# Kernel tuning notes

Hardware: AMD Instinct MI355X
Metric: run time of the kernel (lower is better)

## Reference

```python
import jax, jax.numpy as jnp
import numpy as np

N, E, G = 100000, 1600000, 128
IN_DIM, H, C = 329, 4, 64
NEG_SLOPE = 0.2


def setup_inputs() -> dict:
    key = jax.random.key(0)
    ks = jax.random.split(key, 12)
    x = jax.random.normal(ks[0], (N, IN_DIM), dtype=jnp.float32)
    edge_index = jax.random.randint(ks[1], (2, E), 0, N, dtype=jnp.int64)
    batch = jnp.sort(jax.random.randint(ks[2], (N,), 0, G, dtype=jnp.int64))
    s = 1.0 / np.sqrt(IN_DIM)
    W = jax.random.uniform(ks[3], (IN_DIM, H * C), jnp.float32, -s, s)
    att_src = jax.random.normal(ks[4], (H, C), dtype=jnp.float32) * 0.1
    att_dst = jax.random.normal(ks[5], (H, C), dtype=jnp.float32) * 0.1
    bias = jnp.zeros((C,), jnp.float32)
    s1 = 1.0 / np.sqrt(C)
    w1 = jax.random.uniform(ks[6], (C, 64), jnp.float32, -s1, s1)
    b1 = jnp.zeros((64,), jnp.float32)
    s2 = 1.0 / np.sqrt(64)
    w2 = jax.random.uniform(ks[7], (64, 1), jnp.float32, -s2, s2)
    b2 = jnp.zeros((1,), jnp.float32)
    return {"x": x, "W": W, "att_src": att_src, "att_dst": att_dst,
            "bias": bias, "w1": w1, "b1": b1, "w2": w2, "b2": b2,
            "edge_index": edge_index, "batch": batch}


def reference(x, W, att_src, att_dst, bias, w1, b1, w2, b2, edge_index, batch):
    # --- GATConv (heads=4, concat=False, add_self_loops=True) ---
    xp = (x @ W).reshape(N, H, C)                       # [N,H,C]
    a_src = jnp.einsum('nhc,hc->nh', xp, att_src)       # [N,H]
    a_dst = jnp.einsum('nhc,hc->nh', xp, att_dst)       # [N,H]
    loops = jnp.arange(N, dtype=edge_index.dtype)
    src = jnp.concatenate([edge_index[0], loops])       # [E+N]
    dst = jnp.concatenate([edge_index[1], loops])
    logits = jax.nn.leaky_relu(a_src[src] + a_dst[dst], NEG_SLOPE)  # [E+N,H]
    # segment softmax over edges sharing a destination
    mx = jax.ops.segment_max(logits, dst, num_segments=N)
    ex = jnp.exp(logits - mx[dst])
    denom = jax.ops.segment_sum(ex, dst, num_segments=N)
    alpha = ex / denom[dst]                             # [E+N,H]
    msg = xp[src] * alpha[:, :, None]                   # [E+N,H,C]
    agg = jax.ops.segment_sum(msg, dst, num_segments=N) # [N,H,C]
    h = jax.nn.relu(agg.mean(axis=1) + bias)            # [N,C]
    # --- global mean pool over graphs ---
    counts = jax.ops.segment_sum(jnp.ones((N,), h.dtype), batch, num_segments=G)
    g = jax.ops.segment_sum(h, batch, num_segments=G) / jnp.maximum(counts, 1.0)[:, None]
    # --- head MLP ---
    y = jax.nn.sigmoid(jax.nn.relu(g @ w1 + b1) @ w2 + b2)  # [G,1]
    return y
```

## Files before the change

### kernel.cpp

```cpp
#include <hip/hip_runtime.h>
#include <math.h>

#define N_NODES 100000
#define N_EDGES 1600000
#define N_GRAPHS 128
#define IN_DIM 329
#define NH 4
#define CC 64
#define HC 256
#define NEG_SLOPE 0.2f

#define K_PAD 384
#define M_PAD 100096
#define NBUCK 196
#define BCAP 10240
#define EPB 4096

typedef unsigned short u16;
typedef unsigned char u8;
typedef unsigned int u32;
typedef __attribute__((ext_vector_type(8))) short short8;
typedef __attribute__((ext_vector_type(4))) float floatx4;
typedef __attribute__((ext_vector_type(2))) float floatx2;

__device__ __forceinline__ u16 f2bf(float f) {
    u32 u = __float_as_uint(f);
    u32 r = (u + 0x7FFFu + ((u >> 16) & 1u)) >> 16;
    return (u16)r;
}

__device__ __forceinline__ u8 f2fp8(float f) {
#if __has_builtin(__builtin_amdgcn_cvt_pk_fp8_f32)
    int pk = __builtin_amdgcn_cvt_pk_fp8_f32(f, f, 0, false);
    return (u8)(pk & 0xFF);
#else
    u32 u = __float_as_uint(f);
    u32 sgn = (u >> 24) & 0x80;
    float af = fabsf(f);
    if (af >= 448.f) return (u8)(sgn | 0x7E);
    if (af < 0.015625f) {
        int m = (int)rintf(af * 512.f);
        if (m >= 8) return (u8)(sgn | 0x08);
        return (u8)(sgn | (u32)m);
    }
    u32 au = u & 0x7FFFFFFF;
    u32 r = au + 0x0007FFFFu + ((au >> 20) & 1u);
    u32 e = r >> 23;
    u32 m3 = (r >> 20) & 7;
    int fe = (int)e - 127 + 7;
    if (fe >= 16) return (u8)(sgn | 0x7E);
    return (u8)(sgn | ((u32)fe << 3) | m3);
#endif
}

__device__ __forceinline__ float fp82f_sw(u32 b) {
    u32 s = (b & 0x80u) << 24;
    u32 e = (b >> 3) & 0xF;
    u32 m = b & 7;
    if (e == 0) {
        float v = (float)m * 0.001953125f;
        return (b & 0x80) ? -v : v;
    }
    return __uint_as_float(s | ((e + 120) << 23) | (m << 20));
}

__device__ __forceinline__ floatx4 dec4(int p) {
#if __has_builtin(__builtin_amdgcn_cvt_pk_f32_fp8)
    floatx2 lo = __builtin_amdgcn_cvt_pk_f32_fp8(p, false);
    floatx2 hi = __builtin_amdgcn_cvt_pk_f32_fp8(p, true);
    floatx4 r; r.x = lo.x; r.y = lo.y; r.z = hi.x; r.w = hi.y;
    return r;
#else
    floatx4 r;
    r.x = fp82f_sw(p & 0xFF);  r.y = fp82f_sw((p >> 8) & 0xFF);
    r.z = fp82f_sw((p >> 16) & 0xFF); r.w = fp82f_sw((p >> 24) & 0xFF);
    return r;
#endif
}

__device__ __forceinline__ void async_copy16(const void* g, void* l) {
    __builtin_amdgcn_global_load_lds((const __attribute__((address_space(1))) void*)g,
                                     (__attribute__((address_space(3))) void*)l, 16, 0, 0);
}

__device__ __forceinline__ float sel4(float4 a, int h) {
    float lo = (h & 1) ? a.y : a.x;
    float hi = (h & 1) ? a.w : a.z;
    return (h & 2) ? hi : lo;
}

__global__ __launch_bounds__(256) void convert_kernel(
    const float* __restrict__ x, const float* __restrict__ W,
    u16* __restrict__ xb, u16* __restrict__ WbT)
{
    const int xslots = M_PAD * (K_PAD / 4);
    int t = blockIdx.x * 256 + threadIdx.x;
    if (t < xslots) {
        int row = t / 96;
        int slot = t - row * 96;
        int k0 = slot * 4;
        ushort4 o = {0, 0, 0, 0};
        if (row < N_NODES) {
            const float* xr = x + (size_t)row * IN_DIM + k0;
            if (k0 + 3 < IN_DIM) {
                o.x = f2bf(xr[0]); o.y = f2bf(xr[1]); o.z = f2bf(xr[2]); o.w = f2bf(xr[3]);
            } else {
                if (k0 < IN_DIM)     o.x = f2bf(xr[0]);
                if (k0 + 1 < IN_DIM) o.y = f2bf(xr[1]);
                if (k0 + 2 < IN_DIM) o.z = f2bf(xr[2]);
            }
        }
        *(ushort4*)(xb + (size_t)row * K_PAD + k0) = o;
    } else {
        int i = t - xslots;
        if (i >= HC * 96) return;
        int c = i / 96;
        int slot = i - c * 96;
        int k0 = slot * 4;
        ushort4 o = {0, 0, 0, 0};
        const float* wp = W + c;
        if (k0 < IN_DIM)     o.x = f2bf(wp[(size_t)k0 * HC]);
        if (k0 + 1 < IN_DIM) o.y = f2bf(wp[(size_t)(k0 + 1) * HC]);
        if (k0 + 2 < IN_DIM) o.z = f2bf(wp[(size_t)(k0 + 2) * HC]);
        if (k0 + 3 < IN_DIM) o.w = f2bf(wp[(size_t)(k0 + 3) * HC]);
        *(ushort4*)(WbT + (size_t)c * K_PAD + k0) = o;
    }
}

__global__ __launch_bounds__(256) void gemm_mfma_kernel(
    const u16* __restrict__ xb, const u16* __restrict__ WbT,
    const float* __restrict__ att_src, const float* __restrict__ att_dst,
    u8* __restrict__ xp8, float* __restrict__ a_src, float* __restrict__ a_dst)
{
    __shared__ u16 As[128 * 64];
    __shared__ u16 Bs[128 * 64];

    const int tid = threadIdx.x;
    const int lane = tid & 63;
    const int wave = tid >> 6;
    const int lr = lane & 15;
    const int q = lane >> 4;
    const int row0 = blockIdx.x * 128;
    const int col0 = blockIdx.y * 128;
    const int rm0 = (wave & 1) * 64;
    const int cn0 = (wave >> 1) * 64;

    floatx4 acc[4][4];
#pragma unroll
    for (int i = 0; i < 4; i++)
#pragma unroll
        for (int j = 0; j < 4; j++) {
            acc[i][j].x = 0.f; acc[i][j].y = 0.f; acc[i][j].z = 0.f; acc[i][j].w = 0.f;
        }

    for (int k0 = 0; k0 < K_PAD; k0 += 64) {
#pragma unroll
        for (int t = 0; t < 4; t++) {
            int off = (tid + t * 256) * 16;
            int row = off >> 7;
            int col = off & 127;
            int gcol = col ^ ((row & 7) * 16);
            const char* ga = (const char*)xb + (size_t)(row0 + row) * (K_PAD * 2) + k0 * 2 + gcol;
            async_copy16(ga, (char*)As + off);
            const char* gb = (const char*)WbT + (size_t)(col0 + row) * (K_PAD * 2) + k0 * 2 + gcol;
            async_copy16(gb, (char*)Bs + off);
        }
        __syncthreads();

        short8 af[2][4], bf[2][4];
#pragma unroll
        for (int ks = 0; ks < 2; ks++) {
#pragma unroll
            for (int i = 0; i < 4; i++) {
                int ra = rm0 + i * 16 + lr;
                int ca = (ks * 64 + q * 16) ^ ((ra & 7) * 16);
                af[ks][i] = *(const short8*)((const char*)As + ra * 128 + ca);
                int rb = cn0 + i * 16 + lr;
                int cb = (ks * 64 + q * 16) ^ ((rb & 7) * 16);
                bf[ks][i] = *(const short8*)((const char*)Bs + rb * 128 + cb);
            }
        }
#pragma unroll
        for (int ks = 0; ks < 2; ks++)
#pragma unroll
            for (int i = 0; i < 4; i++)
#pragma unroll
                for (int j = 0; j < 4; j++)
                    acc[i][j] = __builtin_amdgcn_mfma_f32_16x16x32_bf16(af[ks][i], bf[ks][j], acc[i][j], 0, 0, 0);
        __syncthreads();
    }

    const int h_w = (col0 + cn0) >> 6;
    float asj[4], adj[4];
#pragma unroll
    for (int j = 0; j < 4; j++) {
        asj[j] = att_src[h_w * 64 + j * 16 + lr];
        adj[j] = att_dst[h_w * 64 + j * 16 + lr];
    }
#pragma unroll
    for (int i = 0; i < 4; i++) {
        float psv[4] = {0, 0, 0, 0}, pdv[4] = {0, 0, 0, 0};
#pragma unroll
        for (int j = 0; j < 4; j++) {
            int col = col0 + cn0 + j * 16 + lr;
            float v[4] = {acc[i][j].x, acc[i][j].y, acc[i][j].z, acc[i][j].w};
#pragma unroll
            for (int r = 0; r < 4; r++) {
                psv[r] = fmaf(v[r], asj[j], psv[r]);
                pdv[r] = fmaf(v[r], adj[j], pdv[r]);
                int row = row0 + rm0 + i * 16 + q * 4 + r;
                if (row < N_NODES) xp8[(size_t)row * HC + col] = f2fp8(v[r]);
            }
        }
#pragma unroll
        for (int m = 1; m < 16; m <<= 1) {
#pragma unroll
            for (int r = 0; r < 4; r++) {
                psv[r] += __shfl_xor(psv[r], m, 64);
                pdv[r] += __shfl_xor(pdv[r], m, 64);
            }
        }
        if (lr == 0) {
#pragma unroll
            for (int r = 0; r < 4; r++) {
                int row = row0 + rm0 + i * 16 + q * 4 + r;
                if (row < N_NODES) {
                    a_src[row * 4 + h_w] = psv[r];
                    a_dst[row * 4 + h_w] = pdv[r];
                }
            }
        }
    }
}

__global__ __launch_bounds__(256) void bin2_kernel(
    const int* __restrict__ ei, int* __restrict__ bcur, int2* __restrict__ bins)
{
    __shared__ int hist[NBUCK];
    __shared__ int lofs[NBUCK];
    __shared__ int gpos[NBUCK];
    __shared__ int lcur[NBUCK];
    __shared__ int sc[256];
    __shared__ int2 lbuf[EPB];

    const int t = threadIdx.x;
    const int lo = blockIdx.x * EPB;
    const int hi = min(lo + EPB, N_EDGES + N_NODES);

    for (int b = t; b < NBUCK; b += 256) hist[b] = 0;
    __syncthreads();

    for (int i = lo + t; i < hi; i += 256) {
        int d = (i < N_EDGES) ? ei[N_EDGES + i] : (i - N_EDGES);
        atomicAdd(&hist[d >> 9], 1);
    }
    __syncthreads();

    int v = (t < NBUCK) ? hist[t] : 0;
    sc[t] = v;
    __syncthreads();
    for (int off = 1; off < 256; off <<= 1) {
        int u = (t >= off) ? sc[t - off] : 0;
        __syncthreads();
        sc[t] += u;
        __syncthreads();
    }
    if (t < NBUCK) {
        int excl = sc[t] - v;
        lofs[t] = excl;
        lcur[t] = excl;
        gpos[t] = atomicAdd(&bcur[t], v);
    }
    __syncthreads();

    for (int i = lo + t; i < hi; i += 256) {
        int s, d;
        if (i < N_EDGES) { s = ei[i]; d = ei[N_EDGES + i]; }
        else             { s = i - N_EDGES; d = s; }
        int b = d >> 9;
        int pos = atomicAdd(&lcur[b], 1);
        int2 r; r.x = s; r.y = d;
        lbuf[pos] = r;
    }
    __syncthreads();

    int total = hi - lo;
    for (int i = t; i < total; i += 256) {
        int2 r = lbuf[i];
        int b = r.y >> 9;
        int ob = gpos[b] + (i - lofs[b]);
        if (ob < BCAP) bins[(size_t)b * BCAP + ob] = r;
    }
}

__global__ __launch_bounds__(256) void fill3_kernel(
    const int* __restrict__ bcur, const int2* __restrict__ bins,
    int2* __restrict__ rs_deg, int* __restrict__ csr)
{
    __shared__ int deg[512];
    __shared__ int cur[512];
    __shared__ int sc[256];
    __shared__ int order[BCAP];

    const int t = threadIdx.x;
    const int b = blockIdx.x;
    const int cnt = min(bcur[b], BCAP);
    const int2* bp = bins + (size_t)b * BCAP;
    const int gbase = b * BCAP;

    deg[t] = 0; deg[t + 256] = 0;
    __syncthreads();
    for (int i = t; i < cnt; i += 256) atomicAdd(&deg[bp[i].y & 511], 1);
    __syncthreads();

    int d0 = deg[2 * t], d1 = deg[2 * t + 1];
    sc[t] = d0 + d1;
    __syncthreads();
    for (int off = 1; off < 256; off <<= 1) {
        int u = (t >= off) ? sc[t - off] : 0;
        __syncthreads();
        sc[t] += u;
        __syncthreads();
    }
    int excl = sc[t] - (d0 + d1);
    cur[2 * t] = excl;
    cur[2 * t + 1] = excl + d0;
    int n0 = b * 512 + 2 * t;
    if (n0 < N_NODES)     { int2 rd; rd.x = gbase + excl;      rd.y = d0; rs_deg[n0] = rd; }
    if (n0 + 1 < N_NODES) { int2 rd; rd.x = gbase + excl + d0; rd.y = d1; rs_deg[n0 + 1] = rd; }
    __syncthreads();

    for (int i = t; i < cnt; i += 256) {
        int2 r = bp[i];
        int pos = atomicAdd(&cur[r.y & 511], 1);
        order[pos] = r.x;
    }
    __syncthreads();

    for (int i = t; i < cnt; i += 256) csr[gbase + i] = order[i];
}

__global__ __launch_bounds__(256) void aggregate_kernel(
    const u8* __restrict__ xp8, const float* __restrict__ a_src, const float* __restrict__ a_dst,
    const int2* __restrict__ rs_deg, const int* __restrict__ csr,
    const float* __restrict__ bias, float* __restrict__ hbuf)
{
    int n = blockIdx.x * 4 + (threadIdx.x >> 6);
    int lane = threadIdx.x & 63;
    if (n >= N_NODES) return;
    int2 rd = rs_deg[n];
    int rstart = __builtin_amdgcn_readfirstlane(rd.x);
    int deg    = __builtin_amdgcn_readfirstlane(rd.y);
    const int* ep = csr + rstart;
    int h = lane >> 4;

    float ad = a_dst[n * 4 + h];
    const u8* xpl = xp8 + lane * 4;

    float acc0 = 0.f, acc1 = 0.f, acc2 = 0.f, acc3 = 0.f, den = 0.f;
    int e = 0;
    for (; e + 4 <= deg; e += 4) {
        int s0 = ep[e], s1 = ep[e + 1], s2 = ep[e + 2], s3 = ep[e + 3];
        float4 A0 = *(const float4*)(a_src + s0 * 4);
        float4 A1 = *(const float4*)(a_src + s1 * 4);
        float4 A2 = *(const float4*)(a_src + s2 * 4);
        float4 A3 = *(const float4*)(a_src + s3 * 4);
        int p0 = *(const int*)(xpl + (size_t)s0 * HC);
        int p1 = *(const int*)(xpl + (size_t)s1 * HC);
        int p2 = *(const int*)(xpl + (size_t)s2 * HC);
        int p3 = *(const int*)(xpl + (size_t)s3 * HC);
        float z0 = sel4(A0, h) + ad, z1 = sel4(A1, h) + ad;
        float z2 = sel4(A2, h) + ad, z3 = sel4(A3, h) + ad;
        float w0 = __expf(fmaxf(z0, NEG_SLOPE * z0));
        float w1 = __expf(fmaxf(z1, NEG_SLOPE * z1));
        float w2 = __expf(fmaxf(z2, NEG_SLOPE * z2));
        float w3 = __expf(fmaxf(z3, NEG_SLOPE * z3));
        den += (w0 + w1) + (w2 + w3);
        floatx4 v0 = dec4(p0), v1 = dec4(p1), v2 = dec4(p2), v3 = dec4(p3);
        acc0 = fmaf(w0, v0.x, acc0); acc1 = fmaf(w0, v0.y, acc1);
        acc2 = fmaf(w0, v0.z, acc2); acc3 = fmaf(w0, v0.w, acc3);
        acc0 = fmaf(w1, v1.x, acc0); acc1 = fmaf(w1, v1.y, acc1);
        acc2 = fmaf(w1, v1.z, acc2); acc3 = fmaf(w1, v1.w, acc3);
        acc0 = fmaf(w2, v2.x, acc0); acc1 = fmaf(w2, v2.y, acc1);
        acc2 = fmaf(w2, v2.z, acc2); acc3 = fmaf(w2, v2.w, acc3);
        acc0 = fmaf(w3, v3.x, acc0); acc1 = fmaf(w3, v3.y, acc1);
        acc2 = fmaf(w3, v3.z, acc2); acc3 = fmaf(w3, v3.w, acc3);
    }
    for (; e < deg; e++) {
        int s0 = ep[e];
        float4 A0 = *(const float4*)(a_src + s0 * 4);
        int p0 = *(const int*)(xpl + (size_t)s0 * HC);
        float z0 = sel4(A0, h) + ad;
        float w0 = __expf(fmaxf(z0, NEG_SLOPE * z0));
        den += w0;
        floatx4 v0 = dec4(p0);
        acc0 = fmaf(w0, v0.x, acc0); acc1 = fmaf(w0, v0.y, acc1);
        acc2 = fmaf(w0, v0.z, acc2); acc3 = fmaf(w0, v0.w, acc3);
    }

    float r = 1.f / den;
    acc0 *= r; acc1 *= r; acc2 *= r; acc3 *= r;
#pragma unroll
    for (int m = 16; m <= 32; m <<= 1) {
        acc0 += __shfl_xor(acc0, m, 64);
        acc1 += __shfl_xor(acc1, m, 64);
        acc2 += __shfl_xor(acc2, m, 64);
        acc3 += __shfl_xor(acc3, m, 64);
    }
    if (lane < 16) {
        const float* bp = bias + lane * 4;
        float4 o;
        o.x = fmaxf(0.25f * acc0 + bp[0], 0.f);
        o.y = fmaxf(0.25f * acc1 + bp[1], 0.f);
        o.z = fmaxf(0.25f * acc2 + bp[2], 0.f);
        o.w = fmaxf(0.25f * acc3 + bp[3], 0.f);
        *(float4*)&hbuf[(size_t)n * CC + lane * 4] = o;
    }
}

__global__ __launch_bounds__(256) void pool_mlp_kernel(
    const float* __restrict__ hbuf, const int* __restrict__ batch,
    const float* __restrict__ w1, const float* __restrict__ b1,
    const float* __restrict__ w2, const float* __restrict__ b2,
    float* __restrict__ out)
{
    int g = blockIdx.x;
    int tid = threadIdx.x;
    int lane = tid & 63;
    int w = tid >> 6;
    __shared__ int sb[2];
    __shared__ float red[4][64];
    __shared__ float gv[64];
    if (tid < 2) {
        int target = g + tid;
        int lo = 0, hi = N_NODES;
        while (lo < hi) {
            int mid = (lo + hi) >> 1;
            if (batch[mid] < target) lo = mid + 1; else hi = mid;
        }
        sb[tid] = lo;
    }
    __syncthreads();
    int start = sb[0], end = sb[1];
    int cnt = end - start;
    float sum = 0.f;
    for (int i = start + w; i < end; i += 4) sum += hbuf[(size_t)i * CC + lane];
    red[w][lane] = sum;
    __syncthreads();
    if (tid < 64) {
        float tot = red[0][lane] + red[1][lane] + red[2][lane] + red[3][lane];
        gv[lane] = tot / (float)max(cnt, 1);
    }
    __syncthreads();
    if (tid < 64) {
        float hid = b1[lane];
        for (int c = 0; c < 64; c++) hid = fmaf(gv[c], w1[c * 64 + lane], hid);
        hid = fmaxf(hid, 0.f);
        float part = hid * w2[lane];
#pragma unroll
        for (int off = 32; off > 0; off >>= 1) part += __shfl_xor(part, off, 64);
        if (lane == 0) out[g] = 1.f / (1.f + __expf(-(part + b2[0])));
    }
}

extern "C" void kernel_launch(void* const* d_in, const int* in_sizes, int n_in,
                              void* d_out, int out_size, void* d_ws, size_t ws_size,
                              hipStream_t stream)
{
    const float* x       = (const float*)d_in[0];
    const float* W       = (const float*)d_in[1];
    const float* att_src = (const float*)d_in[2];
    const float* att_dst = (const float*)d_in[3];
    const float* bias    = (const float*)d_in[4];
    const float* w1      = (const float*)d_in[5];
    const float* b1      = (const float*)d_in[6];
    const float* w2      = (const float*)d_in[7];
    const float* b2      = (const float*)d_in[8];
    const int*   ei      = (const int*)d_in[9];
    const int*   batch   = (const int*)d_in[10];
    float* out = (float*)d_out;

    char* ws = (char*)d_ws;
    size_t off = 0;
    auto alloc = [&](size_t bytes) -> void* {
        void* p = ws + off;
        off += (bytes + 255) & ~(size_t)255;
        return p;
    };
    u16*   xb        = (u16*)alloc((size_t)M_PAD * K_PAD * 2);
    u16*   WbT       = (u16*)alloc((size_t)HC * K_PAD * 2);
    u8*    xp8       = (u8*)alloc((size_t)N_NODES * HC);
    float* a_src_b   = (float*)alloc((size_t)N_NODES * NH * 4);
    float* a_dst_b   = (float*)alloc((size_t)N_NODES * NH * 4);
    int*   bcur      = (int*)alloc((size_t)NBUCK * 4);
    int2*  bins      = (int2*)alloc((size_t)NBUCK * BCAP * 8);
    int2*  rs_deg    = (int2*)alloc((size_t)N_NODES * 8);
    int*   csr       = (int*)alloc((size_t)NBUCK * BCAP * 4);
    float* hbuf      = (float*)xb;

    hipMemsetAsync(bcur, 0, (size_t)NBUCK * 4, stream);

    const int xslots = M_PAD * (K_PAD / 4);
    convert_kernel<<<(xslots + HC * 96 + 255) / 256, 256, 0, stream>>>(x, W, xb, WbT);

    dim3 ggrid(M_PAD / 128, 2);
    gemm_mfma_kernel<<<ggrid, 256, 0, stream>>>(xb, WbT, att_src, att_dst,
                                                xp8, a_src_b, a_dst_b);

    int tot = N_EDGES + N_NODES;
    bin2_kernel<<<(tot + EPB - 1) / EPB, 256, 0, stream>>>(ei, bcur, bins);
    fill3_kernel<<<NBUCK, 256, 0, stream>>>(bcur, bins, rs_deg, csr);

    aggregate_kernel<<<(N_NODES + 3) / 4, 256, 0, stream>>>(xp8, a_src_b, a_dst_b,
                                                            rs_deg, csr, bias, hbuf);

    pool_mlp_kernel<<<N_GRAPHS, 256, 0, stream>>>(hbuf, batch, w1, b1, w2, b2, out);
}
```

Before: 463.5 us.

## Fuse x bf16 conversion into GEMM, split attention scores, restructure binning and pooling

The GEMM now reads fp32 x directly into LDS via async copies and converts to bf16 while building fragments, which drops the separate conversion pass and the padded bf16 copy of x. The attention dot products move to a new kernel that reads back the fp8 features and pre-scales by log2(e) so aggregation can use exp2. Binning writes straight to global bins without a local staging sort, with a larger edges-per-block constant. The CSR fill uses 512 threads, and pooling becomes a parallel atomic partial-sum pass followed by a small MLP kernel. Trade-offs: attention logits are now computed from fp8-quantized features, the binned writes are less coalesced, and fp32 atomics make the pooled sums order-dependent.

```diff
diff --git a/kernel.cpp b/kernel.cpp
--- a/kernel.cpp
+++ b/kernel.cpp
@@ -9,12 +9,14 @@
 #define CC 64
 #define HC 256
 #define NEG_SLOPE 0.2f
+#define LOG2E 1.44269504f
 
 #define K_PAD 384
 #define M_PAD 100096
+#define XBYTES (N_NODES * IN_DIM * 4)
 #define NBUCK 196
 #define BCAP 10240
-#define EPB 4096
+#define EPB 8192
 
 typedef unsigned short u16;
 typedef unsigned char u8;
@@ -27,6 +29,10 @@
     u32 u = __float_as_uint(f);
     u32 r = (u + 0x7FFFu + ((u >> 16) & 1u)) >> 16;
     return (u16)r;
+}
+
+__device__ __forceinline__ u32 pkbf(float a, float b) {
+    return __builtin_amdgcn_perm(__float_as_uint(b), __float_as_uint(a), 0x07060302u);
 }
 
 __device__ __forceinline__ u8 f2fp8(float f) {
@@ -89,50 +95,25 @@
     return (h & 2) ? hi : lo;
 }
 
-__global__ __launch_bounds__(256) void convert_kernel(
-    const float* __restrict__ x, const float* __restrict__ W,
-    u16* __restrict__ xb, u16* __restrict__ WbT)
-{
-    const int xslots = M_PAD * (K_PAD / 4);
-    int t = blockIdx.x * 256 + threadIdx.x;
-    if (t < xslots) {
-        int row = t / 96;
-        int slot = t - row * 96;
-        int k0 = slot * 4;
-        ushort4 o = {0, 0, 0, 0};
-        if (row < N_NODES) {
-            const float* xr = x + (size_t)row * IN_DIM + k0;
-            if (k0 + 3 < IN_DIM) {
-                o.x = f2bf(xr[0]); o.y = f2bf(xr[1]); o.z = f2bf(xr[2]); o.w = f2bf(xr[3]);
-            } else {
-                if (k0 < IN_DIM)     o.x = f2bf(xr[0]);
-                if (k0 + 1 < IN_DIM) o.y = f2bf(xr[1]);
-                if (k0 + 2 < IN_DIM) o.z = f2bf(xr[2]);
-            }
-        }
-        *(ushort4*)(xb + (size_t)row * K_PAD + k0) = o;
-    } else {
-        int i = t - xslots;
-        if (i >= HC * 96) return;
-        int c = i / 96;
-        int slot = i - c * 96;
-        int k0 = slot * 4;
-        ushort4 o = {0, 0, 0, 0};
-        const float* wp = W + c;
-        if (k0 < IN_DIM)     o.x = f2bf(wp[(size_t)k0 * HC]);
-        if (k0 + 1 < IN_DIM) o.y = f2bf(wp[(size_t)(k0 + 1) * HC]);
-        if (k0 + 2 < IN_DIM) o.z = f2bf(wp[(size_t)(k0 + 2) * HC]);
-        if (k0 + 3 < IN_DIM) o.w = f2bf(wp[(size_t)(k0 + 3) * HC]);
-        *(ushort4*)(WbT + (size_t)c * K_PAD + k0) = o;
-    }
+__global__ __launch_bounds__(256) void convw_kernel(const float* __restrict__ W, u16* __restrict__ WbT)
+{
+    int i = blockIdx.x * 256 + threadIdx.x;
+    if (i >= HC * 96) return;
+    int c = i / 96;
+    int k0 = (i - c * 96) * 4;
+    ushort4 o = {0, 0, 0, 0};
+    const float* wp = W + c;
+    if (k0 < IN_DIM)     o.x = f2bf(wp[(size_t)k0 * HC]);
+    if (k0 + 1 < IN_DIM) o.y = f2bf(wp[(size_t)(k0 + 1) * HC]);
+    if (k0 + 2 < IN_DIM) o.z = f2bf(wp[(size_t)(k0 + 2) * HC]);
+    if (k0 + 3 < IN_DIM) o.w = f2bf(wp[(size_t)(k0 + 3) * HC]);
+    *(ushort4*)(WbT + (size_t)c * K_PAD + k0) = o;
 }
 
 __global__ __launch_bounds__(256) void gemm_mfma_kernel(
-    const u16* __restrict__ xb, const u16* __restrict__ WbT,
-    const float* __restrict__ att_src, const float* __restrict__ att_dst,
-    u8* __restrict__ xp8, float* __restrict__ a_src, float* __restrict__ a_dst)
-{
-    __shared__ u16 As[128 * 64];
+    const float* __restrict__ x, const u16* __restrict__ WbT, u8* __restrict__ xp8)
+{
+    __shared__ float Asf[128 * 64];
     __shared__ u16 Bs[128 * 64];
 
     const int tid = threadIdx.x;
@@ -155,13 +136,20 @@
 
     for (int k0 = 0; k0 < K_PAD; k0 += 64) {
 #pragma unroll
+        for (int t = 0; t < 8; t++) {
+            int chunk = tid + t * 256;
+            int row = chunk >> 4, ch = chunk & 15;
+            int chl = ch ^ (row & 15);
+            long gb = (long)(row0 + row) * (IN_DIM * 4) + (long)k0 * 4 + chl * 16;
+            if (gb > (long)XBYTES - 16) gb = (long)XBYTES - 16;
+            async_copy16((const char*)x + gb, (char*)Asf + (size_t)chunk * 16);
+        }
+#pragma unroll
         for (int t = 0; t < 4; t++) {
             int off = (tid + t * 256) * 16;
             int row = off >> 7;
             int col = off & 127;
             int gcol = col ^ ((row & 7) * 16);
-            const char* ga = (const char*)xb + (size_t)(row0 + row) * (K_PAD * 2) + k0 * 2 + gcol;
-            async_copy16(ga, (char*)As + off);
             const char* gb = (const char*)WbT + (size_t)(col0 + row) * (K_PAD * 2) + k0 * 2 + gcol;
             async_copy16(gb, (char*)Bs + off);
         }
@@ -173,8 +161,18 @@
 #pragma unroll
             for (int i = 0; i < 4; i++) {
                 int ra = rm0 + i * 16 + lr;
-                int ca = (ks * 64 + q * 16) ^ ((ra & 7) * 16);
-                af[ks][i] = *(const short8*)((const char*)As + ra * 128 + ca);
+                int c0 = ks * 8 + q * 2;
+                int sw = ra & 15;
+                const float4* base = (const float4*)(Asf + ra * 64);
+                float4 lo = base[c0 ^ sw];
+                float4 hi = base[(c0 ^ sw) ^ 1];
+                union { short8 v; u32 w[4]; } fr;
+                fr.w[0] = pkbf(lo.x, lo.y);
+                fr.w[1] = pkbf(lo.z, lo.w);
+                fr.w[2] = pkbf(hi.x, hi.y);
+                fr.w[3] = pkbf(hi.z, hi.w);
+                af[ks][i] = fr.v;
+
                 int rb = cn0 + i * 16 + lr;
                 int cb = (ks * 64 + q * 16) ^ ((rb & 7) * 16);
                 bf[ks][i] = *(const short8*)((const char*)Bs + rb * 128 + cb);
@@ -190,46 +188,44 @@
         __syncthreads();
     }
 
-    const int h_w = (col0 + cn0) >> 6;
-    float asj[4], adj[4];
-#pragma unroll
-    for (int j = 0; j < 4; j++) {
-        asj[j] = att_src[h_w * 64 + j * 16 + lr];
-        adj[j] = att_dst[h_w * 64 + j * 16 + lr];
-    }
 #pragma unroll
     for (int i = 0; i < 4; i++) {
-        float psv[4] = {0, 0, 0, 0}, pdv[4] = {0, 0, 0, 0};
 #pragma unroll
         for (int j = 0; j < 4; j++) {
             int col = col0 + cn0 + j * 16 + lr;
             float v[4] = {acc[i][j].x, acc[i][j].y, acc[i][j].z, acc[i][j].w};
 #pragma unroll
             for (int r = 0; r < 4; r++) {
-                psv[r] = fmaf(v[r], asj[j], psv[r]);
-                pdv[r] = fmaf(v[r], adj[j], pdv[r]);
                 int row = row0 + rm0 + i * 16 + q * 4 + r;
                 if (row < N_NODES) xp8[(size_t)row * HC + col] = f2fp8(v[r]);
             }
         }
-#pragma unroll
-        for (int m = 1; m < 16; m <<= 1) {
-#pragma unroll
-            for (int r = 0; r < 4; r++) {
-                psv[r] += __shfl_xor(psv[r], m, 64);
-                pdv[r] += __shfl_xor(pdv[r], m, 64);
-            }
-        }
-        if (lr == 0) {
-#pragma unroll
-            for (int r = 0; r < 4; r++) {
-                int row = row0 + rm0 + i * 16 + q * 4 + r;
-                if (row < N_NODES) {
-                    a_src[row * 4 + h_w] = psv[r];
-                    a_dst[row * 4 + h_w] = pdv[r];
-                }
-            }
-        }
+    }
+}
+
+__global__ __launch_bounds__(256) void a8_kernel(
+    const u8* __restrict__ xp8, const float* __restrict__ att_src, const float* __restrict__ att_dst,
+    float* __restrict__ a_src, float* __restrict__ a_dst)
+{
+    int n = blockIdx.x * 4 + (threadIdx.x >> 6);
+    int lane = threadIdx.x & 63;
+    if (n >= N_NODES) return;
+    int h = lane >> 4;
+    int c0 = (lane & 15) * 4;
+    int p = *(const int*)(xp8 + (size_t)n * HC + h * CC + c0);
+    floatx4 v = dec4(p);
+    const float* as = att_src + h * CC + c0;
+    const float* ad = att_dst + h * CC + c0;
+    float ps = v.x * as[0] + v.y * as[1] + v.z * as[2] + v.w * as[3];
+    float pd = v.x * ad[0] + v.y * ad[1] + v.z * ad[2] + v.w * ad[3];
+#pragma unroll
+    for (int m = 1; m < 16; m <<= 1) {
+        ps += __shfl_xor(ps, m, 64);
+        pd += __shfl_xor(pd, m, 64);
+    }
+    if ((lane & 15) == 0) {
+        a_src[n * 4 + h] = ps * LOG2E;
+        a_dst[n * 4 + h] = pd * LOG2E;
     }
 }
 
@@ -237,11 +233,9 @@
     const int* __restrict__ ei, int* __restrict__ bcur, int2* __restrict__ bins)
 {
     __shared__ int hist[NBUCK];
-    __shared__ int lofs[NBUCK];
     __shared__ int gpos[NBUCK];
     __shared__ int lcur[NBUCK];
     __shared__ int sc[256];
-    __shared__ int2 lbuf[EPB];
 
     const int t = threadIdx.x;
     const int lo = blockIdx.x * EPB;
@@ -257,20 +251,8 @@
     __syncthreads();
 
     int v = (t < NBUCK) ? hist[t] : 0;
-    sc[t] = v;
-    __syncthreads();
-    for (int off = 1; off < 256; off <<= 1) {
-        int u = (t >= off) ? sc[t - off] : 0;
-        __syncthreads();
-        sc[t] += u;
-        __syncthreads();
-    }
-    if (t < NBUCK) {
-        int excl = sc[t] - v;
-        lofs[t] = excl;
-        lcur[t] = excl;
-        gpos[t] = atomicAdd(&bcur[t], v);
-    }
+    if (t < NBUCK) { gpos[t] = atomicAdd(&bcur[t], v); lcur[t] = 0; }
+    (void)sc;
     __syncthreads();
 
     for (int i = lo + t; i < hi; i += 256) {
@@ -278,22 +260,15 @@
         if (i < N_EDGES) { s = ei[i]; d = ei[N_EDGES + i]; }
         else             { s = i - N_EDGES; d = s; }
         int b = d >> 9;
-        int pos = atomicAdd(&lcur[b], 1);
-        int2 r; r.x = s; r.y = d;
-        lbuf[pos] = r;
-    }
-    __syncthreads();
-
-    int total = hi - lo;
-    for (int i = t; i < total; i += 256) {
-        int2 r = lbuf[i];
-        int b = r.y >> 9;
-        int ob = gpos[b] + (i - lofs[b]);
-        if (ob < BCAP) bins[(size_t)b * BCAP + ob] = r;
-    }
-}
-
-__global__ __launch_bounds__(256) void fill3_kernel(
+        int pos = gpos[b] + atomicAdd(&lcur[b], 1);
+        if (pos < BCAP) {
+            int2 r; r.x = s; r.y = d;
+            bins[(size_t)b * BCAP + pos] = r;
+        }
+    }
+}
+
+__global__ __launch_bounds__(512) void fill3_kernel(
     const int* __restrict__ bcur, const int2* __restrict__ bins,
     int2* __restrict__ rs_deg, int* __restrict__ csr)
 {
@@ -308,36 +283,41 @@
     const int2* bp = bins + (size_t)b * BCAP;
     const int gbase = b * BCAP;
 
-    deg[t] = 0; deg[t + 256] = 0;
-    __syncthreads();
-    for (int i = t; i < cnt; i += 256) atomicAdd(&deg[bp[i].y & 511], 1);
-    __syncthreads();
-
-    int d0 = deg[2 * t], d1 = deg[2 * t + 1];
-    sc[t] = d0 + d1;
+    deg[t] = 0;
+    __syncthreads();
+    for (int i = t; i < cnt; i += 512) atomicAdd(&deg[bp[i].y & 511], 1);
+    __syncthreads();
+
+    int d0 = 0, d1 = 0;
+    if (t < 256) {
+        d0 = deg[2 * t]; d1 = deg[2 * t + 1];
+        sc[t] = d0 + d1;
+    }
     __syncthreads();
     for (int off = 1; off < 256; off <<= 1) {
-        int u = (t >= off) ? sc[t - off] : 0;
+        int u = (t < 256 && t >= off) ? sc[t - off] : 0;
         __syncthreads();
-        sc[t] += u;
+        if (t < 256) sc[t] += u;
         __syncthreads();
     }
-    int excl = sc[t] - (d0 + d1);
-    cur[2 * t] = excl;
-    cur[2 * t + 1] = excl + d0;
-    int n0 = b * 512 + 2 * t;
-    if (n0 < N_NODES)     { int2 rd; rd.x = gbase + excl;      rd.y = d0; rs_deg[n0] = rd; }
-    if (n0 + 1 < N_NODES) { int2 rd; rd.x = gbase + excl + d0; rd.y = d1; rs_deg[n0 + 1] = rd; }
-    __syncthreads();
-
-    for (int i = t; i < cnt; i += 256) {
+    if (t < 256) {
+        int excl = sc[t] - (d0 + d1);
+        cur[2 * t] = excl;
+        cur[2 * t + 1] = excl + d0;
+        int n0 = b * 512 + 2 * t;
+        if (n0 < N_NODES)     { int2 rd; rd.x = gbase + excl;      rd.y = d0; rs_deg[n0] = rd; }
+        if (n0 + 1 < N_NODES) { int2 rd; rd.x = gbase + excl + d0; rd.y = d1; rs_deg[n0 + 1] = rd; }
+    }
+    __syncthreads();
+
+    for (int i = t; i < cnt; i += 512) {
         int2 r = bp[i];
         int pos = atomicAdd(&cur[r.y & 511], 1);
         order[pos] = r.x;
     }
     __syncthreads();
 
-    for (int i = t; i < cnt; i += 256) csr[gbase + i] = order[i];
+    for (int i = t; i < cnt; i += 512) csr[gbase + i] = order[i];
 }
 
 __global__ __launch_bounds__(256) void aggregate_kernel(
@@ -353,9 +333,9 @@
     int deg    = __builtin_amdgcn_readfirstlane(rd.y);
     const int* ep = csr + rstart;
     int h = lane >> 4;
+    int xoff = lane * 4;
 
     float ad = a_dst[n * 4 + h];
-    const u8* xpl = xp8 + lane * 4;
 
     float acc0 = 0.f, acc1 = 0.f, acc2 = 0.f, acc3 = 0.f, den = 0.f;
     int e = 0;
@@ -365,16 +345,16 @@
         float4 A1 = *(const float4*)(a_src + s1 * 4);
         float4 A2 = *(const float4*)(a_src + s2 * 4);
         float4 A3 = *(const float4*)(a_src + s3 * 4);
-        int p0 = *(const int*)(xpl + (size_t)s0 * HC);
-        int p1 = *(const int*)(xpl + (size_t)s1 * HC);
-        int p2 = *(const int*)(xpl + (size_t)s2 * HC);
-        int p3 = *(const int*)(xpl + (size_t)s3 * HC);
+        int p0 = *(const int*)(xp8 + s0 * HC + xoff);
+        int p1 = *(const int*)(xp8 + s1 * HC + xoff);
+        int p2 = *(const int*)(xp8 + s2 * HC + xoff);
+        int p3 = *(const int*)(xp8 + s3 * HC + xoff);
         float z0 = sel4(A0, h) + ad, z1 = sel4(A1, h) + ad;
         float z2 = sel4(A2, h) + ad, z3 = sel4(A3, h) + ad;
-        float w0 = __expf(fmaxf(z0, NEG_SLOPE * z0));
-        float w1 = __expf(fmaxf(z1, NEG_SLOPE * z1));
-        float w2 = __expf(fmaxf(z2, NEG_SLOPE * z2));
-        float w3 = __expf(fmaxf(z3, NEG_SLOPE * z3));
+        float w0 = exp2f(fmaxf(z0, NEG_SLOPE * z0));
+        float w1 = exp2f(fmaxf(z1, NEG_SLOPE * z1));
+        float w2 = exp2f(fmaxf(z2, NEG_SLOPE * z2));
+        float w3 = exp2f(fmaxf(z3, NEG_SLOPE * z3));
         den += (w0 + w1) + (w2 + w3);
         floatx4 v0 = dec4(p0), v1 = dec4(p1), v2 = dec4(p2), v3 = dec4(p3);
         acc0 = fmaf(w0, v0.x, acc0); acc1 = fmaf(w0, v0.y, acc1);
@@ -389,9 +369,9 @@
     for (; e < deg; e++) {
         int s0 = ep[e];
         float4 A0 = *(const float4*)(a_src + s0 * 4);
-        int p0 = *(const int*)(xpl + (size_t)s0 * HC);
+        int p0 = *(const int*)(xp8 + s0 * HC + xoff);
         float z0 = sel4(A0, h) + ad;
-        float w0 = __expf(fmaxf(z0, NEG_SLOPE * z0));
+        float w0 = exp2f(fmaxf(z0, NEG_SLOPE * z0));
         den += w0;
         floatx4 v0 = dec4(p0);
         acc0 = fmaf(w0, v0.x, acc0); acc1 = fmaf(w0, v0.y, acc1);
@@ -418,49 +398,49 @@
     }
 }
 
-__global__ __launch_bounds__(256) void pool_mlp_kernel(
+__global__ __launch_bounds__(256) void pool1_kernel(
     const float* __restrict__ hbuf, const int* __restrict__ batch,
+    float* __restrict__ gsum, int* __restrict__ gcnt)
+{
+    int w = threadIdx.x >> 6, lane = threadIdx.x & 63;
+    int r0 = blockIdx.x * 128 + w * 32;
+    if (r0 >= N_NODES) return;
+    int r1 = min(r0 + 32, N_NODES);
+    int cur = batch[r0];
+    float s = 0.f;
+    int c = 0;
+    for (int r = r0; r < r1; r++) {
+        int bb = batch[r];
+        if (bb != cur) {
+            atomicAdd(&gsum[cur * 64 + lane], s);
+            if (lane == 0) atomicAdd(&gcnt[cur], c);
+            s = 0.f; c = 0; cur = bb;
+        }
+        s += hbuf[(size_t)r * CC + lane];
+        c++;
+    }
+    atomicAdd(&gsum[cur * 64 + lane], s);
+    if (lane == 0) atomicAdd(&gcnt[cur], c);
+}
+
+__global__ __launch_bounds__(64) void pool2_kernel(
+    const float* __restrict__ gsum, const int* __restrict__ gcnt,
     const float* __restrict__ w1, const float* __restrict__ b1,
     const float* __restrict__ w2, const float* __restrict__ b2,
     float* __restrict__ out)
 {
     int g = blockIdx.x;
-    int tid = threadIdx.x;
-    int lane = tid & 63;
-    int w = tid >> 6;
-    __shared__ int sb[2];
-    __shared__ float red[4][64];
+    int lane = threadIdx.x;
     __shared__ float gv[64];
-    if (tid < 2) {
-        int target = g + tid;
-        int lo = 0, hi = N_NODES;
-        while (lo < hi) {
-            int mid = (lo + hi) >> 1;
-            if (batch[mid] < target) lo = mid + 1; else hi = mid;
-        }
-        sb[tid] = lo;
-    }
-    __syncthreads();
-    int start = sb[0], end = sb[1];
-    int cnt = end - start;
-    float sum = 0.f;
-    for (int i = start + w; i < end; i += 4) sum += hbuf[(size_t)i * CC + lane];
-    red[w][lane] = sum;
-    __syncthreads();
-    if (tid < 64) {
-        float tot = red[0][lane] + red[1][lane] + red[2][lane] + red[3][lane];
-        gv[lane] = tot / (float)max(cnt, 1);
-    }
-    __syncthreads();
-    if (tid < 64) {
-        float hid = b1[lane];
-        for (int c = 0; c < 64; c++) hid = fmaf(gv[c], w1[c * 64 + lane], hid);
-        hid = fmaxf(hid, 0.f);
-        float part = hid * w2[lane];
-#pragma unroll
-        for (int off = 32; off > 0; off >>= 1) part += __shfl_xor(part, off, 64);
-        if (lane == 0) out[g] = 1.f / (1.f + __expf(-(part + b2[0])));
-    }
+    gv[lane] = gsum[g * 64 + lane] / (float)max(gcnt[g], 1);
+    __syncthreads();
+    float hid = b1[lane];
+    for (int c = 0; c < 64; c++) hid = fmaf(gv[c], w1[c * 64 + lane], hid);
+    hid = fmaxf(hid, 0.f);
+    float part = hid * w2[lane];
+#pragma unroll
+    for (int off = 32; off > 0; off >>= 1) part += __shfl_xor(part, off, 64);
+    if (lane == 0) out[g] = 1.f / (1.f + __expf(-(part + b2[0])));
 }
 
 extern "C" void kernel_launch(void* const* d_in, const int* in_sizes, int n_in,
@@ -487,32 +467,36 @@
         off += (bytes + 255) & ~(size_t)255;
         return p;
     };
-    u16*   xb        = (u16*)alloc((size_t)M_PAD * K_PAD * 2);
     u16*   WbT       = (u16*)alloc((size_t)HC * K_PAD * 2);
     u8*    xp8       = (u8*)alloc((size_t)N_NODES * HC);
     float* a_src_b   = (float*)alloc((size_t)N_NODES * NH * 4);
     float* a_dst_b   = (float*)alloc((size_t)N_NODES * NH * 4);
+    size_t zoff0 = off;
     int*   bcur      = (int*)alloc((size_t)NBUCK * 4);
+    float* gsum      = (float*)alloc((size_t)N_GRAPHS * 64 * 4);
+    int*   gcnt      = (int*)alloc((size_t)N_GRAPHS * 4);
+    size_t zbytes = off - zoff0;
     int2*  bins      = (int2*)alloc((size_t)NBUCK * BCAP * 8);
     int2*  rs_deg    = (int2*)alloc((size_t)N_NODES * 8);
     int*   csr       = (int*)alloc((size_t)NBUCK * BCAP * 4);
-    float* hbuf      = (float*)xb;
-
-    hipMemsetAsync(bcur, 0, (size_t)NBUCK * 4, stream);
-
-    const int xslots = M_PAD * (K_PAD / 4);
-    convert_kernel<<<(xslots + HC * 96 + 255) / 256, 256, 0, stream>>>(x, W, xb, WbT);
+    float* hbuf      = (float*)alloc((size_t)N_NODES * CC * 4);
+
+    hipMemsetAsync(bcur, 0, zbytes, stream);
+
+    convw_kernel<<<(HC * 96 + 255) / 256, 256, 0, stream>>>(W, WbT);
 
     dim3 ggrid(M_PAD / 128, 2);
-    gemm_mfma_kernel<<<ggrid, 256, 0, stream>>>(xb, WbT, att_src, att_dst,
-                                                xp8, a_src_b, a_dst_b);
+    gemm_mfma_kernel<<<ggrid, 256, 0, stream>>>(x, WbT, xp8);
+
+    a8_kernel<<<(N_NODES + 3) / 4, 256, 0, stream>>>(xp8, att_src, att_dst, a_src_b, a_dst_b);
 
     int tot = N_EDGES + N_NODES;
     bin2_kernel<<<(tot + EPB - 1) / EPB, 256, 0, stream>>>(ei, bcur, bins);
-    fill3_kernel<<<NBUCK, 256, 0, stream>>>(bcur, bins, rs_deg, csr);
+    fill3_kernel<<<NBUCK, 512, 0, stream>>>(bcur, bins, rs_deg, csr);
 
     aggregate_kernel<<<(N_NODES + 3) / 4, 256, 0, stream>>>(xp8, a_src_b, a_dst_b,
                                                             rs_deg, csr, bias, hbuf);
 
-    pool_mlp_kernel<<<N_GRAPHS, 256, 0, stream>>>(hbuf, batch, w1, b1, w2, b2, out);
-}
+    pool1_kernel<<<(N_NODES + 127) / 128, 256, 0, stream>>>(hbuf, batch, gsum, gcnt);
+    pool2_kernel<<<N_GRAPHS, 64, 0, stream>>>(gsum, gcnt, w1, b1, w2, b2, out);
+}
```

New measurement: 427.9 us. 1.08x faster.
